# Optimization experiments

Hardware: AMD Instinct MI355X
Metric: run time of the kernel (lower is better)

## Reference

```python
import jax, jax.numpy as jnp
import numpy as np

NUM_HEADS = 6
EPS = 1e-6

def setup_inputs() -> dict:
    key = jax.random.key(0)
    k1, k2, k3, k4, k5 = jax.random.split(key, 5)
    B, N, C = 8, 1024, 384
    x = jax.random.normal(k1, (B, N, C), dtype=jnp.float32)
    # torch nn.Linear weights stored here as [in, out] for y = x @ W
    w_qkv = jax.random.normal(k2, (C, 3 * C), dtype=jnp.float32) * 0.02
    w_out = jax.random.normal(k3, (C, C), dtype=jnp.float32) * 0.02
    b_out = jax.random.normal(k4, (C,), dtype=jnp.float32) * 0.02
    # non-negative random-walk visitation mask (avg visits per node)
    mask = jax.random.uniform(k5, (N, N), dtype=jnp.float32)
    return {"x": x, "w_qkv": w_qkv, "w_out": w_out, "b_out": b_out, "mask": mask}

def reference(x, w_qkv, w_out, b_out, mask):
    B, N, C = x.shape
    H = NUM_HEADS
    D = C // H
    qkv = x @ w_qkv                                   # [B,N,3C]
    q, k, v = jnp.split(qkv, 3, axis=-1)
    # [B,N,C] -> [B,H,N,D]
    to_heads = lambda t: t.reshape(B, N, H, D).transpose(0, 2, 1, 3)
    q, k, v = to_heads(q), to_heads(k), to_heads(v)
    # feature map: relu(x) + eps
    q = jax.nn.relu(q) + EPS
    k = jax.nn.relu(k) + EPS
    # masked linear kernel: (Phi(Q) Phi(K)^T * mask)
    kernel = jnp.einsum("bhnd,bhmd->bhnm", q, k) * mask  # [B,H,N,N]
    z = 1.0 / (kernel.sum(axis=-1, keepdims=True) + EPS)  # row normalizer
    out = jnp.einsum("bhnm,bhmd->bhnd", kernel, v) * z    # [B,H,N,D]
    out = out.transpose(0, 2, 1, 3).reshape(B, N, C)
    return out @ w_out + b_out
```

## Files before the change

kernel.cpp:

```cpp
#include <hip/hip_runtime.h>
#include <hip/hip_bf16.h>
#include <hip/hip_fp16.h>
#include <stdint.h>

typedef __hip_bfloat16 bf16;
typedef __attribute__((ext_vector_type(8))) short short8;
typedef __attribute__((ext_vector_type(4))) float f32x4;
typedef __attribute__((ext_vector_type(16))) float f32x16;
typedef __attribute__((ext_vector_type(4))) int int4v;
typedef __attribute__((ext_vector_type(4))) unsigned short ushort4v;

#define MFMA16(A,B,C) __builtin_amdgcn_mfma_f32_16x16x32_bf16(A,B,C,0,0,0)
#define MFMA32(A,B,C) __builtin_amdgcn_mfma_f32_32x32x16_bf16(A,B,C,0,0,0)

#define FENCE() asm volatile("" ::: "memory")
#define SBAR()  do { FENCE(); __builtin_amdgcn_s_barrier(); FENCE(); } while (0)
#define WAITVN(N) asm volatile("s_waitcnt vmcnt(" #N ")" ::: "memory")

static __device__ __forceinline__ void g2lds16(const void* g, void* l) {
  __builtin_amdgcn_global_load_lds(
      (__attribute__((address_space(1))) void*)(g),
      (__attribute__((address_space(3))) void*)(l), 16, 0, 0);
}

static __device__ __forceinline__ int swz8(int row, int kc) {
  return row * 8 + (kc ^ (row & 7));
}

static __device__ __forceinline__ unsigned short f2bf_bits(float f) {
  bf16 t = __float2bfloat16(f); unsigned short u; __builtin_memcpy(&u, &t, 2); return u;
}
static __device__ __forceinline__ unsigned short f2h_bits(float f) {
  __half t = __float2half(f); unsigned short u; __builtin_memcpy(&u, &t, 2); return u;
}

template<bool HALFOUT>
static __device__ __forceinline__ void tileT(const float* __restrict__ in,
                                             unsigned short* __restrict__ out,
                                             int R, int C, int tr, int tc, int tid,
                                             float (*tls)[65]) {
  const int rr0 = tid >> 4, c4 = tid & 15;
  #pragma unroll
  for (int rr = 0; rr < 4; ++rr) {
    int r = rr0 + rr * 16;
    float4 v = *(const float4*)(in + (size_t)(tr * 64 + r) * C + tc * 64 + c4 * 4);
    tls[r][c4 * 4 + 0] = v.x; tls[r][c4 * 4 + 1] = v.y;
    tls[r][c4 * 4 + 2] = v.z; tls[r][c4 * 4 + 3] = v.w;
  }
  __syncthreads();
  #pragma unroll
  for (int rr = 0; rr < 4; ++rr) {
    int r2 = rr0 + rr * 16;
    ushort4v o;
    #pragma unroll
    for (int k = 0; k < 4; ++k) {
      float f = tls[c4 * 4 + k][r2];
      o[k] = HALFOUT ? f2h_bits(f) : f2bf_bits(f);
    }
    *(ushort4v*)(out + (size_t)(tc * 64 + r2) * R + tr * 64 + c4 * 4) = o;
  }
}

__global__ __launch_bounds__(256)
void k_prep(const float* __restrict__ x, bf16* __restrict__ xb,
            const float* __restrict__ wqkv, unsigned short* __restrict__ wqkvT,
            const float* __restrict__ wout, unsigned short* __restrict__ woutT,
            const float* __restrict__ mask, unsigned short* __restrict__ maskT) {
  __shared__ float tls[64][65];
  const int bid = blockIdx.x, tid = threadIdx.x;
  if (bid < 768) {
    #pragma unroll
    for (int j = 0; j < 4; ++j) {
      int i = bid * 1024 + j * 256 + tid;
      float4 v = ((const float4*)x)[i];
      bf16* po = xb + (size_t)i * 4;
      po[0] = __float2bfloat16(v.x); po[1] = __float2bfloat16(v.y);
      po[2] = __float2bfloat16(v.z); po[3] = __float2bfloat16(v.w);
    }
  } else if (bid < 876) {
    int tt = bid - 768; tileT<false>(wqkv, wqkvT, 384, 1152, tt / 18, tt % 18, tid, tls);
  } else if (bid < 912) {
    int tt = bid - 876; tileT<false>(wout, woutT, 384, 384, tt / 6, tt % 6, tid, tls);
  } else {
    int tt = bid - 912; tileT<true>(mask, maskT, 1024, 1024, tt / 16, tt % 16, tid, tls);
  }
}

template<int EPI>
__global__ __launch_bounds__(256, 2)
void k_gemm(const bf16* __restrict__ A, const bf16* __restrict__ BT,
            bf16* __restrict__ Cb, float* __restrict__ Cf,
            const float* __restrict__ bias, bf16* __restrict__ vT,
            int M, int N, int K)
{
  __shared__ __align__(16) bf16 As[128 * 64];
  __shared__ __align__(16) bf16 Bs[128 * 64];
  const int tid = threadIdx.x;
  const int wave = tid >> 6, lane = tid & 63;
  const int lhi = lane >> 4, llo = lane & 15;
  const int wr = wave >> 1, wc = wave & 1;
  const int mBase = blockIdx.x * 128, nBase = blockIdx.y * 128;

  f32x4 acc[4][4] = {};

  for (int kt = 0; kt < K; kt += 64) {
    __syncthreads();
    for (int i = 0; i < 4; ++i) {
      int c = (wave * 4 + i) * 64 + lane;
      int row = c >> 3;
      int kc = (c & 7) ^ (row & 7);
      g2lds16(A  + (size_t)(mBase + row) * K + kt + kc * 8, As + (c & ~63) * 8);
      g2lds16(BT + (size_t)(nBase + row) * K + kt + kc * 8, Bs + (c & ~63) * 8);
    }
    __syncthreads();
    for (int kk = 0; kk < 2; ++kk) {
      const int kc = kk * 4 + lhi;
      short8 a[4], b[4];
      for (int mi = 0; mi < 4; ++mi)
        a[mi] = *(const short8*)(As + swz8(wr * 64 + mi * 16 + llo, kc) * 8);
      for (int ni = 0; ni < 4; ++ni)
        b[ni] = *(const short8*)(Bs + swz8(wc * 64 + ni * 16 + llo, kc) * 8);
      for (int mi = 0; mi < 4; ++mi)
        for (int ni = 0; ni < 4; ++ni)
          acc[mi][ni] = MFMA16(a[mi], b[ni], acc[mi][ni]);
    }
  }

  for (int mi = 0; mi < 4; ++mi)
    for (int ni = 0; ni < 4; ++ni) {
      const int colbase = nBase + wc * 64 + ni * 16;
      if (EPI == 1) {
        for (int j = 0; j < 4; ++j) {
          int row = mBase + wr * 64 + mi * 16 + lhi * 4 + j;
          int col = colbase + llo;
          Cf[(size_t)row * N + col] = acc[mi][ni][j] + bias[col];
        }
      } else if (colbase < 768) {
        for (int j = 0; j < 4; ++j) {
          int row = mBase + wr * 64 + mi * 16 + lhi * 4 + j;
          int col = colbase + llo;
          float v = fmaxf(acc[mi][ni][j], 0.f) + 1e-6f;
          Cb[(size_t)row * N + col] = __float2bfloat16(v);
        }
      } else {
        int col = colbase + llo;
        int dall = col - 768, hh = dall >> 6, dd = dall & 63;
        int rowg = mBase + wr * 64 + mi * 16 + lhi * 4;
        int bb = rowg >> 10, nloc = rowg & 1023;
        ushort4v pk;
        for (int j = 0; j < 4; ++j) pk[j] = f2bf_bits(acc[mi][ni][j]);
        *(ushort4v*)((unsigned short*)vT + (((size_t)bb * 6 + hh) * 64 + dd) * 1024 + nloc) = pk;
      }
    }
}

__global__ __launch_bounds__(256, 3)
void k_attn(const bf16* __restrict__ qkv,
            const bf16* __restrict__ vT,
            const __half* __restrict__ maskT,
            bf16* __restrict__ out)
{
  __shared__ __align__(16) bf16 Ks[2][64 * 64];
  __shared__ __align__(16) bf16 Vs[2][64 * 64];
  __shared__ float Ored[2][32][65];
  __shared__ float zred[2][2][32];

  const int bid = blockIdx.x;
  const int bh = bid % 48, qt = bid / 48;
  const int b = bh / 6, h = bh - b * 6;
  const int tid = threadIdx.x, wave = tid >> 6, lane = tid & 63;
  const int lq = lane & 31, lh = lane >> 5;
  const int wq = wave & 1, wm = wave >> 1;
  const size_t row0 = (size_t)b * 1024;
  const int qglob = qt * 64 + wq * 32 + lq;

  auto stageKV = [&](int mt, int buf) {
    #pragma unroll
    for (int i = 0; i < 2; ++i) {
      int c = (wave * 2 + i) * 64 + lane;
      int row = c >> 3;
      int kc = (c & 7) ^ (row & 7);
      g2lds16(qkv + (row0 + mt * 64 + row) * 1152 + 384 + h * 64 + kc * 8,
              Ks[buf] + (c & ~63) * 8);
      g2lds16(vT + ((size_t)bh * 64 + row) * 1024 + mt * 64 + kc * 8,
              Vs[buf] + (c & ~63) * 8);
    }
  };

  short8 bq[4];
  {
    const bf16* qp = qkv + (row0 + qglob) * 1152 + h * 64 + lh * 8;
    #pragma unroll
    for (int ks = 0; ks < 4; ++ks) bq[ks] = *(const short8*)(qp + ks * 16);
  }
  stageKV(0, 0);

  f32x16 accO[2] = {};
  float zl = 0.f;

  #pragma unroll 1
  for (int mt = 0; mt < 16; ++mt) {
    const int cur = mt & 1;
    const bf16* Kc = Ks[cur];
    const bf16* Vc = Vs[cur];

    __half mv[16];
    {
      const int mrow0 = mt * 64 + wm * 32 + 4 * lh;
      #pragma unroll
      for (int g = 0; g < 4; ++g)
        #pragma unroll
        for (int j = 0; j < 4; ++j)
          mv[g * 4 + j] = maskT[(size_t)(mrow0 + 8 * g + j) * 1024 + qglob];
    }
    if (mt < 15) {
      stageKV(mt + 1, cur ^ 1);
      WAITVN(20);
    } else {
      WAITVN(16);
    }
    SBAR();

    f32x16 st = {};
    #pragma unroll
    for (int ks = 0; ks < 4; ++ks) {
      int row = wm * 32 + lq;
      int cc = (ks * 2 + lh) ^ (row & 7);
      short8 af = *(const short8*)(Kc + (row * 8 + cc) * 8);
      st = MFMA32(af, bq[ks], st);
    }

    float p[16];
    {
      float zp = 0.f;
      #pragma unroll
      for (int r = 0; r < 16; ++r) {
        p[r] = st[r] * __half2float(mv[r]);
        zp += p[r];
      }
      zl += zp;
    }
    int u[4][2];
    #pragma unroll
    for (int g = 0; g < 4; ++g)
      #pragma unroll
      for (int c = 0; c < 2; ++c)
        asm("v_cvt_pk_bf16_f32 %0, %1, %2"
            : "=v"(u[g][c]) : "v"(p[4 * g + 2 * c]), "v"(p[4 * g + 2 * c + 1]));

    short8 pa[2];
    #pragma unroll
    for (int ks = 0; ks < 2; ++ks) {
      int A0 = u[2 * ks][0], A0b = u[2 * ks][1];
      int A1 = u[2 * ks + 1][0], A1b = u[2 * ks + 1][1];
      int x0 = __shfl_xor(A0, 32), x1 = __shfl_xor(A0b, 32);
      int y0 = __shfl_xor(A1, 32), y1 = __shfl_xor(A1b, 32);
      int4v iv;
      iv.x = lh ? y0 : A0;
      iv.y = lh ? y1 : A0b;
      iv.z = lh ? A1 : x0;
      iv.w = lh ? A1b : x1;
      pa[ks] = *(short8*)&iv;
    }

    #pragma unroll
    for (int db = 0; db < 2; ++db)
      #pragma unroll
      for (int ks = 0; ks < 2; ++ks) {
        int row = db * 32 + lq;
        int cc = (wm * 4 + ks * 2 + lh) ^ (row & 7);
        short8 vb = *(const short8*)(Vc + (row * 8 + cc) * 8);
        accO[db] = MFMA32(pa[ks], vb, accO[db]);
      }

    SBAR();
  }

  zl += __shfl_xor(zl, 32);
  zred[wq][wm][lq] = zl;
  if (wm == 1) {
    #pragma unroll
    for (int db = 0; db < 2; ++db)
      #pragma unroll
      for (int r = 0; r < 16; ++r) {
        int q = (r & 3) + 8 * (r >> 2) + 4 * lh;
        Ored[wq][q][db * 32 + lq] = accO[db][r];
      }
  }
  __syncthreads();
  if (wm == 0) {
    #pragma unroll
    for (int r = 0; r < 16; ++r) {
      int q = (r & 3) + 8 * (r >> 2) + 4 * lh;
      float zt = zred[wq][0][q] + zred[wq][1][q];
      float zi = 1.f / (zt + 1e-6f);
      int n = qt * 64 + wq * 32 + q;
      size_t orow = (row0 + n) * 384 + h * 64;
      #pragma unroll
      for (int db = 0; db < 2; ++db) {
        float val = (accO[db][r] + Ored[wq][q][db * 32 + lq]) * zi;
        out[orow + db * 32 + lq] = __float2bfloat16(val);
      }
    }
  }
}

__global__ __launch_bounds__(256, 3)
void k_gemm_out(const bf16* __restrict__ A, const bf16* __restrict__ BT,
                float* __restrict__ Cf, const float* __restrict__ bias)
{
  __shared__ __align__(16) bf16 As[64 * 64];
  __shared__ __align__(16) bf16 Bs[64 * 64];
  const int tid = threadIdx.x;
  const int wave = tid >> 6, lane = tid & 63;
  const int lq = lane & 31, lh = lane >> 5;
  const int wr = wave >> 1, wc = wave & 1;
  const int mBase = blockIdx.x * 64, nBase = blockIdx.y * 64;
  const int N = 384, K = 384;

  f32x16 acc = {};
  for (int kt = 0; kt < K; kt += 64) {
    __syncthreads();
    #pragma unroll
    for (int i = 0; i < 2; ++i) {
      int c = (wave * 2 + i) * 64 + lane;
      int row = c >> 3;
      int kc = (c & 7) ^ (row & 7);
      g2lds16(A  + (size_t)(mBase + row) * K + kt + kc * 8, As + (c & ~63) * 8);
      g2lds16(BT + (size_t)(nBase + row) * K + kt + kc * 8, Bs + (c & ~63) * 8);
    }
    __syncthreads();
    #pragma unroll
    for (int ks = 0; ks < 4; ++ks) {
      int ra = wr * 32 + lq, rb = wc * 32 + lq;
      short8 a = *(const short8*)(As + (ra * 8 + ((ks * 2 + lh) ^ (ra & 7))) * 8);
      short8 b = *(const short8*)(Bs + (rb * 8 + ((ks * 2 + lh) ^ (rb & 7))) * 8);
      acc = MFMA32(a, b, acc);
    }
  }
  #pragma unroll
  for (int r = 0; r < 16; ++r) {
    int row = mBase + wr * 32 + (r & 3) + 8 * (r >> 2) + 4 * lh;
    int col = nBase + wc * 32 + lq;
    Cf[(size_t)row * N + col] = acc[r] + bias[col];
  }
}

extern "C" void kernel_launch(void* const* d_in, const int* in_sizes, int n_in,
                              void* d_out, int out_size, void* d_ws, size_t ws_size,
                              hipStream_t stream) {
  (void)in_sizes; (void)n_in; (void)out_size; (void)ws_size;
  const float* x    = (const float*)d_in[0];
  const float* wqkv = (const float*)d_in[1];
  const float* wout = (const float*)d_in[2];
  const float* bout = (const float*)d_in[3];
  const float* mask = (const float*)d_in[4];
  float* outp = (float*)d_out;

  char* ws = (char*)d_ws;
  bf16*  xb    = (bf16*)(ws);
  bf16*  wqkvT = (bf16*)(ws + 6291456);
  bf16*  woutT = (bf16*)(ws + 7176192);
  bf16*  qkvb  = (bf16*)(ws + 7471104);
  bf16*  vTb   = (bf16*)(ws + 26345472);
  bf16*  ab    = (bf16*)(ws + 32636928);
  __half* maskT = (__half*)(ws + 38928384);

  k_prep<<<dim3(1168), dim3(256), 0, stream>>>(
      x, xb, wqkv, (unsigned short*)wqkvT, wout, (unsigned short*)woutT,
      mask, (unsigned short*)maskT);

  k_gemm<0><<<dim3(64, 9), dim3(256), 0, stream>>>(xb, wqkvT, qkvb, nullptr, nullptr,
                                                   vTb, 8192, 1152, 384);
  k_attn<<<dim3(768), dim3(256), 0, stream>>>(qkvb, vTb, maskT, ab);
  k_gemm_out<<<dim3(128, 6), dim3(256), 0, stream>>>(ab, woutT, outp, bout);
}
```

Baseline: 58.81 us.

## Double-buffer LDS tiles in QKV and output GEMMs; simplify attention loop sync

Both GEMM kernels now keep two LDS buffers for the A and B tiles. The next K-tile is issued via global_load_lds before the MFMAs on the current tile, so global load latency can overlap compute. The attention kernel drops its hand-written s_waitcnt vmcnt and raw s_barrier in favour of a single __syncthreads at the end of each iteration, plus one before the loop. That is simpler but gives up the finer-grained wait that let mask loads stay in flight. The GEMMs double their LDS use, which may limit occupancy.

New measurement: 64.96 us. 10.5% more time.

```diff
diff --git a/kernel.cpp b/kernel.cpp
--- a/kernel.cpp
+++ b/kernel.cpp
@@ -12,10 +12,6 @@
 
 #define MFMA16(A,B,C) __builtin_amdgcn_mfma_f32_16x16x32_bf16(A,B,C,0,0,0)
 #define MFMA32(A,B,C) __builtin_amdgcn_mfma_f32_32x32x16_bf16(A,B,C,0,0,0)
-
-#define FENCE() asm volatile("" ::: "memory")
-#define SBAR()  do { FENCE(); __builtin_amdgcn_s_barrier(); FENCE(); } while (0)
-#define WAITVN(N) asm volatile("s_waitcnt vmcnt(" #N ")" ::: "memory")
 
 static __device__ __forceinline__ void g2lds16(const void* g, void* l) {
   __builtin_amdgcn_global_load_lds(
@@ -93,8 +89,8 @@
             const float* __restrict__ bias, bf16* __restrict__ vT,
             int M, int N, int K)
 {
-  __shared__ __align__(16) bf16 As[128 * 64];
-  __shared__ __align__(16) bf16 Bs[128 * 64];
+  __shared__ __align__(16) bf16 As[2][128 * 64];
+  __shared__ __align__(16) bf16 Bs[2][128 * 64];
   const int tid = threadIdx.x;
   const int wave = tid >> 6, lane = tid & 63;
   const int lhi = lane >> 4, llo = lane & 15;
@@ -103,27 +99,39 @@
 
   f32x4 acc[4][4] = {};
 
-  for (int kt = 0; kt < K; kt += 64) {
-    __syncthreads();
+  auto stage = [&](int kt, int buf) {
+    #pragma unroll
     for (int i = 0; i < 4; ++i) {
       int c = (wave * 4 + i) * 64 + lane;
       int row = c >> 3;
       int kc = (c & 7) ^ (row & 7);
-      g2lds16(A  + (size_t)(mBase + row) * K + kt + kc * 8, As + (c & ~63) * 8);
-      g2lds16(BT + (size_t)(nBase + row) * K + kt + kc * 8, Bs + (c & ~63) * 8);
-    }
-    __syncthreads();
+      g2lds16(A  + (size_t)(mBase + row) * K + kt + kc * 8, As[buf] + (c & ~63) * 8);
+      g2lds16(BT + (size_t)(nBase + row) * K + kt + kc * 8, Bs[buf] + (c & ~63) * 8);
+    }
+  };
+
+  const int nT = K >> 6;
+  stage(0, 0);
+  __syncthreads();
+  for (int t = 0; t < nT; ++t) {
+    const int cur = t & 1;
+    if (t + 1 < nT) stage((t + 1) << 6, cur ^ 1);
     for (int kk = 0; kk < 2; ++kk) {
       const int kc = kk * 4 + lhi;
       short8 a[4], b[4];
+      #pragma unroll
       for (int mi = 0; mi < 4; ++mi)
-        a[mi] = *(const short8*)(As + swz8(wr * 64 + mi * 16 + llo, kc) * 8);
+        a[mi] = *(const short8*)(As[cur] + swz8(wr * 64 + mi * 16 + llo, kc) * 8);
+      #pragma unroll
       for (int ni = 0; ni < 4; ++ni)
-        b[ni] = *(const short8*)(Bs + swz8(wc * 64 + ni * 16 + llo, kc) * 8);
+        b[ni] = *(const short8*)(Bs[cur] + swz8(wc * 64 + ni * 16 + llo, kc) * 8);
+      #pragma unroll
       for (int mi = 0; mi < 4; ++mi)
+        #pragma unroll
         for (int ni = 0; ni < 4; ++ni)
           acc[mi][ni] = MFMA16(a[mi], b[ni], acc[mi][ni]);
     }
+    __syncthreads();
   }
 
   for (int mi = 0; mi < 4; ++mi)
@@ -198,6 +206,8 @@
   f32x16 accO[2] = {};
   float zl = 0.f;
 
+  __syncthreads();
+
   #pragma unroll 1
   for (int mt = 0; mt < 16; ++mt) {
     const int cur = mt & 1;
@@ -213,13 +223,7 @@
         for (int j = 0; j < 4; ++j)
           mv[g * 4 + j] = maskT[(size_t)(mrow0 + 8 * g + j) * 1024 + qglob];
     }
-    if (mt < 15) {
-      stageKV(mt + 1, cur ^ 1);
-      WAITVN(20);
-    } else {
-      WAITVN(16);
-    }
-    SBAR();
+    if (mt < 15) stageKV(mt + 1, cur ^ 1);
 
     f32x16 st = {};
     #pragma unroll
@@ -273,7 +277,7 @@
         accO[db] = MFMA32(pa[ks], vb, accO[db]);
       }
 
-    SBAR();
+    __syncthreads();
   }
 
   zl += __shfl_xor(zl, 32);
@@ -309,8 +313,8 @@
 void k_gemm_out(const bf16* __restrict__ A, const bf16* __restrict__ BT,
                 float* __restrict__ Cf, const float* __restrict__ bias)
 {
-  __shared__ __align__(16) bf16 As[64 * 64];
-  __shared__ __align__(16) bf16 Bs[64 * 64];
+  __shared__ __align__(16) bf16 As[2][64 * 64];
+  __shared__ __align__(16) bf16 Bs[2][64 * 64];
   const int tid = threadIdx.x;
   const int wave = tid >> 6, lane = tid & 63;
   const int lq = lane & 31, lh = lane >> 5;
@@ -318,25 +322,32 @@
   const int mBase = blockIdx.x * 64, nBase = blockIdx.y * 64;
   const int N = 384, K = 384;
 
-  f32x16 acc = {};
-  for (int kt = 0; kt < K; kt += 64) {
-    __syncthreads();
+  auto stage = [&](int kt, int buf) {
     #pragma unroll
     for (int i = 0; i < 2; ++i) {
       int c = (wave * 2 + i) * 64 + lane;
       int row = c >> 3;
       int kc = (c & 7) ^ (row & 7);
-      g2lds16(A  + (size_t)(mBase + row) * K + kt + kc * 8, As + (c & ~63) * 8);
-      g2lds16(BT + (size_t)(nBase + row) * K + kt + kc * 8, Bs + (c & ~63) * 8);
-    }
-    __syncthreads();
+      g2lds16(A  + (size_t)(mBase + row) * K + kt + kc * 8, As[buf] + (c & ~63) * 8);
+      g2lds16(BT + (size_t)(nBase + row) * K + kt + kc * 8, Bs[buf] + (c & ~63) * 8);
+    }
+  };
+
+  f32x16 acc = {};
+  const int nT = K >> 6;
+  stage(0, 0);
+  __syncthreads();
+  for (int t = 0; t < nT; ++t) {
+    const int cur = t & 1;
+    if (t + 1 < nT) stage((t + 1) << 6, cur ^ 1);
     #pragma unroll
     for (int ks = 0; ks < 4; ++ks) {
       int ra = wr * 32 + lq, rb = wc * 32 + lq;
-      short8 a = *(const short8*)(As + (ra * 8 + ((ks * 2 + lh) ^ (ra & 7))) * 8);
-      short8 b = *(const short8*)(Bs + (rb * 8 + ((ks * 2 + lh) ^ (rb & 7))) * 8);
+      short8 a = *(const short8*)(As[cur] + (ra * 8 + ((ks * 2 + lh) ^ (ra & 7))) * 8);
+      short8 b = *(const short8*)(Bs[cur] + (rb * 8 + ((ks * 2 + lh) ^ (rb & 7))) * 8);
       acc = MFMA32(a, b, acc);
     }
+    __syncthreads();
   }
   #pragma unroll
   for (int r = 0; r < 16; ++r) {
```
